# Optimization experiments

Hardware: AMD Instinct MI355X
Metric: run time of the kernel (lower is better)

## Reference

```python
import jax, jax.numpy as jnp
import numpy as np

B, S, D = 512, 64, 2048


def setup_inputs() -> dict:
    key = jax.random.key(0)
    ks = jax.random.split(key, 5)
    return {
        "classical_state": jax.random.normal(ks[0], (B, D), jnp.float32),
        "amplitudes": jax.random.normal(ks[1], (S, D), jnp.float32),
        "phases": jax.random.normal(ks[2], (S, D), jnp.float32),
        "rotation_gates": jax.random.normal(ks[3], (S, 2, 2), jnp.float32),
        "entanglement_matrix": jax.random.normal(ks[4], (S, S), jnp.float32),
    }


def reference(classical_state, amplitudes, phases, rotation_gates, entanglement_matrix):
    # classical_state: [B, D]; amplitudes/phases: [S, D]; rotation_gates: [S, 2, 2]
    b, d = classical_state.shape
    s = amplitudes.shape[0]

    # create_superposition
    norm_amp = amplitudes / jnp.linalg.norm(amplitudes, axis=1, keepdims=True)  # F.normalize p=2 dim=1
    real_amp = norm_amp * (jnp.cos(phases) + jnp.sin(phases))                   # [S, D]

    # _apply_quantum_rotation: per-pair (x[:, 2p:2p+2] @ gate) for each gate i -> vectorized over S and pairs
    xr = classical_state.reshape(b, d // 2, 2)                                  # [B, P, 2]
    rotated = jnp.einsum('bpi,sij->bspj', xr, rotation_gates).reshape(b, s, d)  # [B, S, D]

    states = real_amp[None, :, :] * rotated                                     # weighted superposition [B, S, D]

    # _apply_entanglement: softmax over rows then matmul across superposition dim
    ent_w = jax.nn.softmax(entanglement_matrix, axis=1)                          # [S, S]
    entangled = jnp.einsum('st,btd->bsd', ent_w, states)                         # [B, S, D]

    # collapse_superposition: multinomial over softmax(sum of squares), gather selected state
    logits = jnp.sum(entangled * entangled, axis=2)                              # [B, S]
    probabilities = jax.nn.softmax(logits, axis=1)
    outcome = jax.random.categorical(jax.random.key(42), logits, axis=1)         # [B] ~ multinomial(probabilities)
    collapsed = jnp.take_along_axis(entangled, outcome[:, None, None], axis=1)[:, 0, :]  # [B, D]
    return collapsed
```

## Files before the change

kernel.cpp:

```cpp
#include <hip/hip_runtime.h>
#include <math.h>

#define NB 512
#define NS 64
#define ND 2048
#define NP 1024

#define OFF_M0   0
#define OFF_M1   131072
#define OFF_QT   262144
#define OFF_R    458752
#define OFF_W    589824
#define OFF_PART 593920

__device__ __forceinline__ unsigned rotl32(unsigned x, int d) {
    return (x << d) | (x >> (32 - d));
}

__device__ __forceinline__ void threefry2x32(unsigned k0, unsigned k1,
                                             unsigned& x0, unsigned& x1) {
    const unsigned ks0 = k0, ks1 = k1, ks2 = k0 ^ k1 ^ 0x1BD11BDAu;
    const int r0[4] = {13, 15, 26, 6};
    const int r1[4] = {17, 29, 16, 24};
    x0 += ks0; x1 += ks1;
#pragma unroll
    for (int i = 0; i < 4; ++i) { x0 += x1; x1 = rotl32(x1, r0[i]); x1 ^= x0; }
    x0 += ks1; x1 += ks2 + 1u;
#pragma unroll
    for (int i = 0; i < 4; ++i) { x0 += x1; x1 = rotl32(x1, r1[i]); x1 ^= x0; }
    x0 += ks2; x1 += ks0 + 2u;
#pragma unroll
    for (int i = 0; i < 4; ++i) { x0 += x1; x1 = rotl32(x1, r0[i]); x1 ^= x0; }
    x0 += ks0; x1 += ks1 + 3u;
#pragma unroll
    for (int i = 0; i < 4; ++i) { x0 += x1; x1 = rotl32(x1, r1[i]); x1 ^= x0; }
    x0 += ks1; x1 += ks2 + 4u;
#pragma unroll
    for (int i = 0; i < 4; ++i) { x0 += x1; x1 = rotl32(x1, r0[i]); x1 ^= x0; }
    x0 += ks2; x1 += ks0 + 5u;
}

__global__ void __launch_bounds__(256)
k_pre(const float* __restrict__ amp, const float* __restrict__ ph,
      const float* __restrict__ E, float* __restrict__ R,
      float* __restrict__ W) {
    __shared__ float in_sh;
    const int t = blockIdx.x;
    const int tid = threadIdx.x;

    if (tid < 16) {
        const float4* a4 = (const float4*)(amp + t * ND);
        float acc = 0.f;
#pragma unroll 8
        for (int i = 0; i < 32; ++i) {
            float4 v = a4[tid + 16 * i];
            acc += v.x * v.x + v.y * v.y + v.z * v.z + v.w * v.w;
        }
        acc += __shfl_down(acc, 8, 16);
        acc += __shfl_down(acc, 4, 16);
        acc += __shfl_down(acc, 2, 16);
        acc += __shfl_down(acc, 1, 16);
        if (tid == 0) in_sh = 1.0f / sqrtf(acc);
    }
    if (tid >= 64 && tid < 128) {
        const int s = tid - 64;
        float e = E[t * NS + s];
        float m = e;
        for (int off = 32; off; off >>= 1) m = fmaxf(m, __shfl_down(m, off));
        m = __shfl(m, 0);
        float ex = expf(e - m);
        float sum = ex;
        for (int off = 32; off; off >>= 1) sum += __shfl_down(sum, off);
        sum = __shfl(sum, 0);
        W[t * NS + s] = ex / sum;
    }
    __syncthreads();

    const float in = in_sh;
    const float2* a2 = (const float2*)(amp + t * ND);
    const float2* p2 = (const float2*)(ph + t * ND);
    float2* r2 = (float2*)(R + t * ND);
#pragma unroll
    for (int k = 0; k < 4; ++k) {
        const int i = tid + 256 * k;
        float2 av = a2[i], pv = p2[i];
        float2 rv;
        rv.x = av.x * in * (__cosf(pv.x) + __sinf(pv.x));
        rv.y = av.y * in * (__cosf(pv.y) + __sinf(pv.y));
        r2[i] = rv;
    }
}

__global__ void __launch_bounds__(1024)
k_MQ(const float* __restrict__ R, const float* __restrict__ W,
     const float* __restrict__ G,
     float* __restrict__ M0, float* __restrict__ M1, float* __restrict__ Qt) {
    __shared__ float W_l[NS];
    __shared__ float Gl[NS * 4];
    __shared__ float4 part4[4][256];
    const int blk = blockIdx.x;
    const int tid = threadIdx.x;
    const int srow = blk >> 2;

    if (tid < NS) W_l[tid] = W[srow * NS + tid];
    if (tid >= 256 && tid < 256 + NS * 4) Gl[tid - 256] = G[tid - 256];
    __syncthreads();

    {
        const int pi = tid & 255;
        const int tg = tid >> 8;
        const int p = ((blk & 3) << 8) + pi;
        const int t0 = tg << 4;
        const float2* r2 = (const float2*)R;
        float a0 = 0.f, a1 = 0.f, b0 = 0.f, b1 = 0.f;
#pragma unroll 4
        for (int j = 0; j < 16; ++j) {
            const int t = t0 + ((j + srow) & 15);
            float2 rv = r2[t * NP + p];
            float w = W_l[t];
            float wr0 = w * rv.x, wr1 = w * rv.y;
            a0 += wr0 * Gl[4 * t + 0];
            b0 += wr0 * Gl[4 * t + 2];
            a1 += wr1 * Gl[4 * t + 1];
            b1 += wr1 * Gl[4 * t + 3];
        }
        part4[tg][pi] = make_float4(a0, a1, b0, b1);
    }
    __syncthreads();

    if (tid < 256) {
        const int p = ((blk & 3) << 8) + tid;
        float4 s0 = part4[0][tid], s1 = part4[1][tid],
               s2 = part4[2][tid], s3 = part4[3][tid];
        float a0 = s0.x + s1.x + s2.x + s3.x;
        float a1 = s0.y + s1.y + s2.y + s3.y;
        float b0 = s0.z + s1.z + s2.z + s3.z;
        float b1 = s0.w + s1.w + s2.w + s3.w;
        float2 m0v = {a0, a1}, m1v = {b0, b1};
        ((float2*)(M0 + srow * ND))[p] = m0v;
        ((float2*)(M1 + srow * ND))[p] = m1v;
        float* qp = Qt + p * 192 + srow * 3;
        qp[0] = a0 * a0 + a1 * a1;
        qp[1] = a0 * b0 + a1 * b1;
        qp[2] = b0 * b0 + b1 * b1;
    }
}

__global__ void __launch_bounds__(1024)
k_logA(const float* __restrict__ x, const float* __restrict__ Qt,
       float* __restrict__ pglob) {
    __shared__ float4 xq[8][256];
    __shared__ float part[16][8][64];
    const int blk = blockIdx.x;
    const int tid = threadIdx.x;
    const int rg = blk >> 2, pc = blk & 3;
    const int r0 = rg * 8;

    {
        const int r = tid >> 7, i = tid & 127;
        float4 v = ((const float4*)(x + (r0 + r) * ND + pc * 512))[i];
        float4 q0, q1;
        q0.x = v.x * v.x; q0.y = 2.f * v.x * v.y; q0.z = v.y * v.y; q0.w = 0.f;
        q1.x = v.z * v.z; q1.y = 2.f * v.z * v.w; q1.z = v.w * v.w; q1.w = 0.f;
        xq[r][2 * i] = q0;
        xq[r][2 * i + 1] = q1;
    }
    __syncthreads();

    const int w = tid >> 6, s = tid & 63;
    {
        float acc[8] = {0.f, 0.f, 0.f, 0.f, 0.f, 0.f, 0.f, 0.f};
        const float* qbase = Qt + (pc * 256) * 192 + s * 3;
#pragma unroll 4
        for (int j = 0; j < 16; ++j) {
            const int pl = (w << 4) + ((j + rg) & 15);
            const float* qp = qbase + pl * 192;
            float q0 = qp[0], q1 = qp[1], q2 = qp[2];
#pragma unroll
            for (int r = 0; r < 8; ++r) {
                float4 xv = xq[r][pl];
                acc[r] += xv.x * q0 + xv.y * q1 + xv.z * q2;
            }
        }
#pragma unroll
        for (int r = 0; r < 8; ++r) part[w][r][s] = acc[r];
    }
    __syncthreads();

    if (tid < 512) {
        const int rr = tid >> 6;
        float l = 0.f;
#pragma unroll
        for (int k = 0; k < 16; ++k) l += part[k][rr][s];
        pglob[(pc * NB + r0 + rr) * NS + s] = l;
    }
}

__global__ void __launch_bounds__(1024)
k_logB(const float* __restrict__ x, const float* __restrict__ pglob,
       const float* __restrict__ M0, const float* __restrict__ M1,
       float* __restrict__ out) {
    __shared__ float2 xs[2 * NP];
    __shared__ int o_sh[2];
    const int blk = blockIdx.x;
    const int tid = threadIdx.x;
    const int r0 = 2 * blk;

    ((float4*)xs)[tid] = ((const float4*)(x + r0 * ND))[tid];

    if (tid < 128) {
        const int w2 = tid >> 6, s = tid & 63;
        const int row = r0 + w2;
        float l = 0.f;
#pragma unroll
        for (int c = 0; c < 4; ++c) l += pglob[(c * NB + row) * NS + s];
        unsigned n = (unsigned)(row * NS + s);
        unsigned t0u = 0u, t1u = n;
        threefry2x32(0u, 42u, t0u, t1u);
        unsigned bits = t0u ^ t1u;
        float u = (float)(bits >> 9) * (1.0f / 8388608.0f);
        u = fmaxf(u, 1.17549435e-38f);
        float g = -logf(-logf(u));
        float best = l + g;
        int bi = s;
        for (int off = 32; off; off >>= 1) {
            float ov = __shfl_down(best, off);
            int oi = __shfl_down(bi, off);
            if (ov > best || (ov == best && oi < bi)) { best = ov; bi = oi; }
        }
        if (s == 0) o_sh[w2] = bi;
    }
    __syncthreads();

#pragma unroll
    for (int r = 0; r < 2; ++r) {
        const int o = o_sh[r];
        const float2* m0p = (const float2*)(M0 + o * ND);
        const float2* m1p = (const float2*)(M1 + o * ND);
        const float2* xr = xs + r * NP;
        float2* op = (float2*)(out + (r0 + r) * ND);
        float2 xv = xr[tid], m0 = m0p[tid], m1 = m1p[tid];
        float2 rr;
        rr.x = xv.x * m0.x + xv.y * m1.x;
        rr.y = xv.x * m0.y + xv.y * m1.y;
        op[tid] = rr;
    }
}

extern "C" void kernel_launch(void* const* d_in, const int* in_sizes, int n_in,
                              void* d_out, int out_size, void* d_ws, size_t ws_size,
                              hipStream_t stream) {
    const float* x   = (const float*)d_in[0];
    const float* amp = (const float*)d_in[1];
    const float* ph  = (const float*)d_in[2];
    const float* G   = (const float*)d_in[3];
    const float* E   = (const float*)d_in[4];
    float* out = (float*)d_out;
    float* ws = (float*)d_ws;

    float* M0 = ws + OFF_M0;
    float* M1 = ws + OFF_M1;
    float* Qt = ws + OFF_QT;
    float* R  = ws + OFF_R;
    float* W  = ws + OFF_W;
    float* pp = ws + OFF_PART;

    k_pre <<<64, 256, 0, stream>>>(amp, ph, E, R, W);
    k_MQ  <<<256, 1024, 0, stream>>>(R, W, G, M0, M1, Qt);
    k_logA<<<256, 1024, 0, stream>>>(x, Qt, pp);
    k_logB<<<256, 1024, 0, stream>>>(x, pp, M0, M1, out);
}
```

Measured before the change: 84.88 us.

## Transpose R and pad Qt to float4, retile all kernels for more blocks

k_pre now writes the normalized amplitude tensor transposed (pair-major), so k_MQ can read contiguous float4 runs along the superposition index. k_MQ pre-multiplies softmax weights by gates in shared memory and runs as more, smaller blocks. Qt is padded to float4 per entry so k_logA does one vector load per element, and k_logA splits the pair dimension into 8 chunks to double its grid. k_logB handles one row per block with float4 I/O and no shared staging of x. The goal is better coalescing and more parallelism, at the cost of strided transposed writes in k_pre and a larger pglob reduction.

Measured after the change: 87.14 us. 2.7% more time.

```diff
diff --git a/kernel.cpp b/kernel.cpp
--- a/kernel.cpp
+++ b/kernel.cpp
@@ -9,9 +9,9 @@
 #define OFF_M0   0
 #define OFF_M1   131072
 #define OFF_QT   262144
-#define OFF_R    458752
-#define OFF_W    589824
-#define OFF_PART 593920
+#define OFF_RT   524288
+#define OFF_W    655360
+#define OFF_PART 659456
 
 __device__ __forceinline__ unsigned rotl32(unsigned x, int d) {
     return (x << d) | (x >> (32 - d));
@@ -42,7 +42,7 @@
 
 __global__ void __launch_bounds__(256)
 k_pre(const float* __restrict__ amp, const float* __restrict__ ph,
-      const float* __restrict__ E, float* __restrict__ R,
+      const float* __restrict__ E, float* __restrict__ RT,
       float* __restrict__ W) {
     __shared__ float in_sh;
     const int t = blockIdx.x;
@@ -79,7 +79,7 @@
     const float in = in_sh;
     const float2* a2 = (const float2*)(amp + t * ND);
     const float2* p2 = (const float2*)(ph + t * ND);
-    float2* r2 = (float2*)(R + t * ND);
+    float2* rT = (float2*)RT;
 #pragma unroll
     for (int k = 0; k < 4; ++k) {
         const int i = tid + 256 * k;
@@ -87,78 +87,67 @@
         float2 rv;
         rv.x = av.x * in * (__cosf(pv.x) + __sinf(pv.x));
         rv.y = av.y * in * (__cosf(pv.y) + __sinf(pv.y));
-        r2[i] = rv;
-    }
-}
-
-__global__ void __launch_bounds__(1024)
-k_MQ(const float* __restrict__ R, const float* __restrict__ W,
+        rT[(i << 6) + t] = rv;
+    }
+}
+
+__global__ void __launch_bounds__(256)
+k_MQ(const float* __restrict__ RT, const float* __restrict__ W,
      const float* __restrict__ G,
      float* __restrict__ M0, float* __restrict__ M1, float* __restrict__ Qt) {
-    __shared__ float W_l[NS];
-    __shared__ float Gl[NS * 4];
-    __shared__ float4 part4[4][256];
+    __shared__ float WG[NS * 4];
+    __shared__ float4 part4[4][64];
     const int blk = blockIdx.x;
-    const int tid = threadIdx.x;
-    const int srow = blk >> 2;
-
-    if (tid < NS) W_l[tid] = W[srow * NS + tid];
-    if (tid >= 256 && tid < 256 + NS * 4) Gl[tid - 256] = G[tid - 256];
-    __syncthreads();
-
-    {
-        const int pi = tid & 255;
-        const int tg = tid >> 8;
-        const int p = ((blk & 3) << 8) + pi;
-        const int t0 = tg << 4;
-        const float2* r2 = (const float2*)R;
-        float a0 = 0.f, a1 = 0.f, b0 = 0.f, b1 = 0.f;
-#pragma unroll 4
-        for (int j = 0; j < 16; ++j) {
-            const int t = t0 + ((j + srow) & 15);
-            float2 rv = r2[t * NP + p];
-            float w = W_l[t];
-            float wr0 = w * rv.x, wr1 = w * rv.y;
-            a0 += wr0 * Gl[4 * t + 0];
-            b0 += wr0 * Gl[4 * t + 2];
-            a1 += wr1 * Gl[4 * t + 1];
-            b1 += wr1 * Gl[4 * t + 3];
-        }
-        part4[tg][pi] = make_float4(a0, a1, b0, b1);
-    }
-    __syncthreads();
-
-    if (tid < 256) {
-        const int p = ((blk & 3) << 8) + tid;
+    const int srow = blk >> 4, pc = blk & 15;
+    const int tid = threadIdx.x;
+
+    WG[tid] = W[srow * NS + (tid >> 2)] * G[tid];
+    __syncthreads();
+
+    const int pi = tid & 63, tg = tid >> 6;
+    const int p = (pc << 6) + pi;
+    const float4* rt = (const float4*)RT + p * 32 + tg * 8;
+    float a0 = 0.f, a1 = 0.f, b0 = 0.f, b1 = 0.f;
+#pragma unroll
+    for (int i = 0; i < 8; ++i) {
+        float4 rv = rt[i];
+        const int tb = (tg << 6) + (i << 3);
+        a0 += rv.x * WG[tb + 0]; b0 += rv.x * WG[tb + 2];
+        a1 += rv.y * WG[tb + 1]; b1 += rv.y * WG[tb + 3];
+        a0 += rv.z * WG[tb + 4]; b0 += rv.z * WG[tb + 6];
+        a1 += rv.w * WG[tb + 5]; b1 += rv.w * WG[tb + 7];
+    }
+    part4[tg][pi] = make_float4(a0, a1, b0, b1);
+    __syncthreads();
+
+    if (tid < 64) {
         float4 s0 = part4[0][tid], s1 = part4[1][tid],
                s2 = part4[2][tid], s3 = part4[3][tid];
-        float a0 = s0.x + s1.x + s2.x + s3.x;
-        float a1 = s0.y + s1.y + s2.y + s3.y;
-        float b0 = s0.z + s1.z + s2.z + s3.z;
-        float b1 = s0.w + s1.w + s2.w + s3.w;
-        float2 m0v = {a0, a1}, m1v = {b0, b1};
-        ((float2*)(M0 + srow * ND))[p] = m0v;
-        ((float2*)(M1 + srow * ND))[p] = m1v;
-        float* qp = Qt + p * 192 + srow * 3;
-        qp[0] = a0 * a0 + a1 * a1;
-        qp[1] = a0 * b0 + a1 * b1;
-        qp[2] = b0 * b0 + b1 * b1;
+        float A0 = s0.x + s1.x + s2.x + s3.x;
+        float A1 = s0.y + s1.y + s2.y + s3.y;
+        float B0 = s0.z + s1.z + s2.z + s3.z;
+        float B1 = s0.w + s1.w + s2.w + s3.w;
+        const int P = (pc << 6) + tid;
+        ((float2*)(M0 + srow * ND))[P] = make_float2(A0, A1);
+        ((float2*)(M1 + srow * ND))[P] = make_float2(B0, B1);
+        ((float4*)Qt)[P * 64 + srow] =
+            make_float4(A0 * A0 + A1 * A1, A0 * B0 + A1 * B1, B0 * B0 + B1 * B1, 0.f);
     }
 }
 
 __global__ void __launch_bounds__(1024)
 k_logA(const float* __restrict__ x, const float* __restrict__ Qt,
        float* __restrict__ pglob) {
-    __shared__ float4 xq[8][256];
+    __shared__ float4 xq[8][128];
     __shared__ float part[16][8][64];
     const int blk = blockIdx.x;
     const int tid = threadIdx.x;
-    const int rg = blk >> 2, pc = blk & 3;
+    const int rg = blk >> 3, pc = blk & 7;
     const int r0 = rg * 8;
 
-    {
-        const int r = tid >> 7, i = tid & 127;
-        float4 v = ((const float4*)(x + (r0 + r) * ND + pc * 512))[i];
+    if (tid < 512) {
+        const int r = tid >> 6, i = tid & 63;
+        float4 v = ((const float4*)(x + (r0 + r) * ND + pc * 256))[i];
         float4 q0, q1;
         q0.x = v.x * v.x; q0.y = 2.f * v.x * v.y; q0.z = v.y * v.y; q0.w = 0.f;
         q1.x = v.z * v.z; q1.y = 2.f * v.z * v.w; q1.z = v.w * v.w; q1.w = 0.f;
@@ -168,23 +157,21 @@
     __syncthreads();
 
     const int w = tid >> 6, s = tid & 63;
-    {
-        float acc[8] = {0.f, 0.f, 0.f, 0.f, 0.f, 0.f, 0.f, 0.f};
-        const float* qbase = Qt + (pc * 256) * 192 + s * 3;
-#pragma unroll 4
-        for (int j = 0; j < 16; ++j) {
-            const int pl = (w << 4) + ((j + rg) & 15);
-            const float* qp = qbase + pl * 192;
-            float q0 = qp[0], q1 = qp[1], q2 = qp[2];
-#pragma unroll
-            for (int r = 0; r < 8; ++r) {
-                float4 xv = xq[r][pl];
-                acc[r] += xv.x * q0 + xv.y * q1 + xv.z * q2;
-            }
+    float acc[8] = {0.f, 0.f, 0.f, 0.f, 0.f, 0.f, 0.f, 0.f};
+    const float4* qt4 = (const float4*)Qt + (pc * 128 + (w << 3)) * 64 + s;
+#pragma unroll
+    for (int j = 0; j < 8; ++j) {
+        const int jj = (j + rg) & 7;
+        const int pl = (w << 3) + jj;
+        float4 q = qt4[jj * 64];
+#pragma unroll
+        for (int r = 0; r < 8; ++r) {
+            float4 xv = xq[r][pl];
+            acc[r] += xv.x * q.x + xv.y * q.y + xv.z * q.z;
         }
-#pragma unroll
-        for (int r = 0; r < 8; ++r) part[w][r][s] = acc[r];
-    }
+    }
+#pragma unroll
+    for (int r = 0; r < 8; ++r) part[w][r][s] = acc[r];
     __syncthreads();
 
     if (tid < 512) {
@@ -196,25 +183,20 @@
     }
 }
 
-__global__ void __launch_bounds__(1024)
+__global__ void __launch_bounds__(512)
 k_logB(const float* __restrict__ x, const float* __restrict__ pglob,
        const float* __restrict__ M0, const float* __restrict__ M1,
        float* __restrict__ out) {
-    __shared__ float2 xs[2 * NP];
-    __shared__ int o_sh[2];
-    const int blk = blockIdx.x;
-    const int tid = threadIdx.x;
-    const int r0 = 2 * blk;
-
-    ((float4*)xs)[tid] = ((const float4*)(x + r0 * ND))[tid];
-
-    if (tid < 128) {
-        const int w2 = tid >> 6, s = tid & 63;
-        const int row = r0 + w2;
+    __shared__ int o_sh;
+    const int r = blockIdx.x;
+    const int tid = threadIdx.x;
+
+    if (tid < 64) {
+        const int s = tid;
         float l = 0.f;
 #pragma unroll
-        for (int c = 0; c < 4; ++c) l += pglob[(c * NB + row) * NS + s];
-        unsigned n = (unsigned)(row * NS + s);
+        for (int c = 0; c < 8; ++c) l += pglob[(c * NB + r) * NS + s];
+        unsigned n = (unsigned)(r * NS + s);
         unsigned t0u = 0u, t1u = n;
         threefry2x32(0u, 42u, t0u, t1u);
         unsigned bits = t0u ^ t1u;
@@ -228,23 +210,20 @@
             int oi = __shfl_down(bi, off);
             if (ov > best || (ov == best && oi < bi)) { best = ov; bi = oi; }
         }
-        if (s == 0) o_sh[w2] = bi;
-    }
-    __syncthreads();
-
-#pragma unroll
-    for (int r = 0; r < 2; ++r) {
-        const int o = o_sh[r];
-        const float2* m0p = (const float2*)(M0 + o * ND);
-        const float2* m1p = (const float2*)(M1 + o * ND);
-        const float2* xr = xs + r * NP;
-        float2* op = (float2*)(out + (r0 + r) * ND);
-        float2 xv = xr[tid], m0 = m0p[tid], m1 = m1p[tid];
-        float2 rr;
-        rr.x = xv.x * m0.x + xv.y * m1.x;
-        rr.y = xv.x * m0.y + xv.y * m1.y;
-        op[tid] = rr;
-    }
+        if (s == 0) o_sh = bi;
+    }
+    __syncthreads();
+
+    const int o = o_sh;
+    float4 xv = ((const float4*)(x + r * ND))[tid];
+    float4 m0 = ((const float4*)(M0 + o * ND))[tid];
+    float4 m1 = ((const float4*)(M1 + o * ND))[tid];
+    float4 rr;
+    rr.x = xv.x * m0.x + xv.y * m1.x;
+    rr.y = xv.x * m0.y + xv.y * m1.y;
+    rr.z = xv.z * m0.z + xv.w * m1.z;
+    rr.w = xv.z * m0.w + xv.w * m1.w;
+    ((float4*)(out + r * ND))[tid] = rr;
 }
 
 extern "C" void kernel_launch(void* const* d_in, const int* in_sizes, int n_in,
@@ -261,12 +240,12 @@
     float* M0 = ws + OFF_M0;
     float* M1 = ws + OFF_M1;
     float* Qt = ws + OFF_QT;
-    float* R  = ws + OFF_R;
+    float* RT = ws + OFF_RT;
     float* W  = ws + OFF_W;
     float* pp = ws + OFF_PART;
 
-    k_pre <<<64, 256, 0, stream>>>(amp, ph, E, R, W);
-    k_MQ  <<<256, 1024, 0, stream>>>(R, W, G, M0, M1, Qt);
-    k_logA<<<256, 1024, 0, stream>>>(x, Qt, pp);
-    k_logB<<<256, 1024, 0, stream>>>(x, pp, M0, M1, out);
-}
+    k_pre <<<64, 256, 0, stream>>>(amp, ph, E, RT, W);
+    k_MQ  <<<1024, 256, 0, stream>>>(RT, W, G, M0, M1, Qt);
+    k_logA<<<512, 1024, 0, stream>>>(x, Qt, pp);
+    k_logB<<<512, 512, 0, stream>>>(x, pp, M0, M1, out);
+}
```

## Fuse preprocessing into MQ kernel and pad Qt to float4 layout

Applied to the files above, without the earlier changes.

Removes the separate k_pre launch and its R/W workspace. Each k_MQ block now recomputes all 64 amplitude norms, its own softmax row, and the phase modulation inline from amp and ph. Qt is stored as padded float4 so k_logA can read it with one vector load instead of three scalar loads. This saves one launch and the R round-trip through memory. The cost is redundant norm computation in every block (each reads the full amp array) and repeated sin/cos work across blocks.

After: 91.88 us. 8.2% more time.

```diff
diff --git a/kernel.cpp b/kernel.cpp
--- a/kernel.cpp
+++ b/kernel.cpp
@@ -9,9 +9,7 @@
 #define OFF_M0   0
 #define OFF_M1   131072
 #define OFF_QT   262144
-#define OFF_R    458752
-#define OFF_W    589824
-#define OFF_PART 593920
+#define OFF_PART 524288
 
 __device__ __forceinline__ unsigned rotl32(unsigned x, int d) {
     return (x << d) | (x >> (32 - d));
@@ -40,31 +38,38 @@
     x0 += ks2; x1 += ks0 + 5u;
 }
 
-__global__ void __launch_bounds__(256)
-k_pre(const float* __restrict__ amp, const float* __restrict__ ph,
-      const float* __restrict__ E, float* __restrict__ R,
-      float* __restrict__ W) {
-    __shared__ float in_sh;
-    const int t = blockIdx.x;
+__global__ void __launch_bounds__(1024)
+k_MQ(const float* __restrict__ amp, const float* __restrict__ ph,
+     const float* __restrict__ G, const float* __restrict__ E,
+     float* __restrict__ M0, float* __restrict__ M1, float* __restrict__ Qt) {
+    __shared__ float norm2[NS];
+    __shared__ float W_l[NS], in_l[NS];
+    __shared__ float Gl[NS * 4];
+    __shared__ float4 part4[4][256];
+    const int blk = blockIdx.x;
     const int tid = threadIdx.x;
-
-    if (tid < 16) {
-        const float4* a4 = (const float4*)(amp + t * ND);
+    const int srow = blk >> 2;
+
+    {
+        const int r = tid >> 4, sub = tid & 15;
+        const float4* a4 = (const float4*)(amp + r * ND);
         float acc = 0.f;
 #pragma unroll 8
         for (int i = 0; i < 32; ++i) {
-            float4 v = a4[tid + 16 * i];
+            float4 v = a4[sub + 16 * i];
             acc += v.x * v.x + v.y * v.y + v.z * v.z + v.w * v.w;
         }
         acc += __shfl_down(acc, 8, 16);
         acc += __shfl_down(acc, 4, 16);
         acc += __shfl_down(acc, 2, 16);
         acc += __shfl_down(acc, 1, 16);
-        if (tid == 0) in_sh = 1.0f / sqrtf(acc);
-    }
-    if (tid >= 64 && tid < 128) {
-        const int s = tid - 64;
-        float e = E[t * NS + s];
+        if (sub == 0) norm2[r] = acc;
+    }
+    if (tid < NS * 4) Gl[tid] = G[tid];
+    __syncthreads();
+    if (tid < NS) {
+        in_l[tid] = 1.0f / sqrtf(norm2[tid]);
+        float e = E[srow * NS + tid];
         float m = e;
         for (int off = 32; off; off >>= 1) m = fmaxf(m, __shfl_down(m, off));
         m = __shfl(m, 0);
@@ -72,38 +77,8 @@
         float sum = ex;
         for (int off = 32; off; off >>= 1) sum += __shfl_down(sum, off);
         sum = __shfl(sum, 0);
-        W[t * NS + s] = ex / sum;
-    }
-    __syncthreads();
-
-    const float in = in_sh;
-    const float2* a2 = (const float2*)(amp + t * ND);
-    const float2* p2 = (const float2*)(ph + t * ND);
-    float2* r2 = (float2*)(R + t * ND);
-#pragma unroll
-    for (int k = 0; k < 4; ++k) {
-        const int i = tid + 256 * k;
-        float2 av = a2[i], pv = p2[i];
-        float2 rv;
-        rv.x = av.x * in * (__cosf(pv.x) + __sinf(pv.x));
-        rv.y = av.y * in * (__cosf(pv.y) + __sinf(pv.y));
-        r2[i] = rv;
-    }
-}
-
-__global__ void __launch_bounds__(1024)
-k_MQ(const float* __restrict__ R, const float* __restrict__ W,
-     const float* __restrict__ G,
-     float* __restrict__ M0, float* __restrict__ M1, float* __restrict__ Qt) {
-    __shared__ float W_l[NS];
-    __shared__ float Gl[NS * 4];
-    __shared__ float4 part4[4][256];
-    const int blk = blockIdx.x;
-    const int tid = threadIdx.x;
-    const int srow = blk >> 2;
-
-    if (tid < NS) W_l[tid] = W[srow * NS + tid];
-    if (tid >= 256 && tid < 256 + NS * 4) Gl[tid - 256] = G[tid - 256];
+        W_l[tid] = ex / sum;
+    }
     __syncthreads();
 
     {
@@ -111,14 +86,17 @@
         const int tg = tid >> 8;
         const int p = ((blk & 3) << 8) + pi;
         const int t0 = tg << 4;
-        const float2* r2 = (const float2*)R;
+        const float2* a2 = (const float2*)amp;
+        const float2* p2 = (const float2*)ph;
         float a0 = 0.f, a1 = 0.f, b0 = 0.f, b1 = 0.f;
 #pragma unroll 4
-        for (int j = 0; j < 16; ++j) {
-            const int t = t0 + ((j + srow) & 15);
-            float2 rv = r2[t * NP + p];
-            float w = W_l[t];
-            float wr0 = w * rv.x, wr1 = w * rv.y;
+        for (int t = t0; t < t0 + 16; ++t) {
+            float2 av = a2[t * NP + p];
+            float2 pv = p2[t * NP + p];
+            float w = W_l[t], in = in_l[t];
+            float ra0 = av.x * in * (__cosf(pv.x) + __sinf(pv.x));
+            float ra1 = av.y * in * (__cosf(pv.y) + __sinf(pv.y));
+            float wr0 = w * ra0, wr1 = w * ra1;
             a0 += wr0 * Gl[4 * t + 0];
             b0 += wr0 * Gl[4 * t + 2];
             a1 += wr1 * Gl[4 * t + 1];
@@ -136,13 +114,10 @@
         float a1 = s0.y + s1.y + s2.y + s3.y;
         float b0 = s0.z + s1.z + s2.z + s3.z;
         float b1 = s0.w + s1.w + s2.w + s3.w;
-        float2 m0v = {a0, a1}, m1v = {b0, b1};
-        ((float2*)(M0 + srow * ND))[p] = m0v;
-        ((float2*)(M1 + srow * ND))[p] = m1v;
-        float* qp = Qt + p * 192 + srow * 3;
-        qp[0] = a0 * a0 + a1 * a1;
-        qp[1] = a0 * b0 + a1 * b1;
-        qp[2] = b0 * b0 + b1 * b1;
+        ((float2*)(M0 + srow * ND))[p] = make_float2(a0, a1);
+        ((float2*)(M1 + srow * ND))[p] = make_float2(b0, b1);
+        ((float4*)Qt)[p * 64 + srow] =
+            make_float4(a0 * a0 + a1 * a1, a0 * b0 + a1 * b1, b0 * b0 + b1 * b1, 0.f);
     }
 }
 
@@ -170,16 +145,16 @@
     const int w = tid >> 6, s = tid & 63;
     {
         float acc[8] = {0.f, 0.f, 0.f, 0.f, 0.f, 0.f, 0.f, 0.f};
-        const float* qbase = Qt + (pc * 256) * 192 + s * 3;
+        const float4* qt4 = (const float4*)Qt + (pc * 256 + (w << 4)) * 64 + s;
 #pragma unroll 4
         for (int j = 0; j < 16; ++j) {
-            const int pl = (w << 4) + ((j + rg) & 15);
-            const float* qp = qbase + pl * 192;
-            float q0 = qp[0], q1 = qp[1], q2 = qp[2];
+            const int jj = (j + rg) & 15;
+            const int pl = (w << 4) + jj;
+            float4 q = qt4[jj * 64];
 #pragma unroll
             for (int r = 0; r < 8; ++r) {
                 float4 xv = xq[r][pl];
-                acc[r] += xv.x * q0 + xv.y * q1 + xv.z * q2;
+                acc[r] += xv.x * q.x + xv.y * q.y + xv.z * q.z;
             }
         }
 #pragma unroll
@@ -261,12 +236,9 @@
     float* M0 = ws + OFF_M0;
     float* M1 = ws + OFF_M1;
     float* Qt = ws + OFF_QT;
-    float* R  = ws + OFF_R;
-    float* W  = ws + OFF_W;
     float* pp = ws + OFF_PART;
 
-    k_pre <<<64, 256, 0, stream>>>(amp, ph, E, R, W);
-    k_MQ  <<<256, 1024, 0, stream>>>(R, W, G, M0, M1, Qt);
+    k_MQ  <<<256, 1024, 0, stream>>>(amp, ph, G, E, M0, M1, Qt);
     k_logA<<<256, 1024, 0, stream>>>(x, Qt, pp);
     k_logB<<<256, 1024, 0, stream>>>(x, pp, M0, M1, out);
 }
```
